# Kernel tuning notes

Hardware: AMD Instinct MI355X
Metric: run time of the kernel (lower is better)

## Reference

```python
import jax, jax.numpy as jnp
import numpy as np

W = 128    # window_size
NH = 8     # num_heads (hard-coded default in ArrowAttention/BiSPA)
NEG = -1e9


def _split_qkv(Wqkv, bqkv):
    Wq, Wk, Wv = jnp.split(Wqkv, 3, axis=1)
    bq, bk, bv = jnp.split(bqkv, 3)
    return (Wq, bq), (Wk, bk), (Wv, bv)


def cls_mha(x, Wqkv, bqkv, Wo, bo):
    # torch nn.MultiheadAttention with query = cls token, key = value = full sequence
    B, S, H = x.shape
    hd = H // NH
    (Wq, bq), (Wk, bk), (Wv, bv) = _split_qkv(Wqkv, bqkv)
    q = (x[:, :1] @ Wq + bq).reshape(B, 1, NH, hd)
    k = (x @ Wk + bk).reshape(B, S, NH, hd)
    v = (x @ Wv + bv).reshape(B, S, NH, hd)
    scores = jnp.einsum('bqhd,bkhd->bhqk', q, k) / jnp.sqrt(jnp.float32(hd))
    attn = jax.nn.softmax(scores, axis=-1)
    out = jnp.einsum('bhqk,bkhd->bqhd', attn, v).reshape(B, 1, H)
    return out @ Wo + bo


def windowed_mha(x, Wqkv, bqkv, Wo, bo, min_key):
    # Fused sliding-window MHA: token i attends to keys j with
    # max(min_key, i-W) <= j <= min(S-1, i+W). Implemented with a 3-block
    # banded layout instead of the original per-token Python loop of MHA calls.
    B, S, H = x.shape
    hd = H // NH
    (Wq, bq), (Wk, bk), (Wv, bv) = _split_qkv(Wqkv, bqkv)
    nb = (S + W - 1) // W
    Sp = nb * W
    pad = Sp - S

    def blk(t):  # [B,S,H] -> [B,nb,W,NH,hd]
        return jnp.pad(t, ((0, 0), (0, pad), (0, 0))).reshape(B, nb, W, NH, hd)

    qb = blk(x @ Wq + bq)
    kb = blk(x @ Wk + bk)
    vb = blk(x @ Wv + bv)

    def ctx(t):  # prev | cur | next block -> [B,nb,3W,NH,hd]
        tp = jnp.pad(t, ((0, 0), (1, 1), (0, 0), (0, 0), (0, 0)))
        return jnp.concatenate([tp[:, :-2], tp[:, 1:-1], tp[:, 2:]], axis=2)

    kc = ctx(kb)
    vc = ctx(vb)
    scores = jnp.einsum('bnqhd,bnkhd->bhnqk', qb, kc) / jnp.sqrt(jnp.float32(hd))
    # global positions of queries / context keys
    qpos = (jnp.arange(nb) * W)[:, None, None] + jnp.arange(W)[None, :, None]          # [nb,W,1]
    kpos = (jnp.arange(nb) * W - W)[:, None, None] + jnp.arange(3 * W)[None, None, :]  # [nb,1,3W]
    rel = kpos - qpos
    valid = (jnp.abs(rel) <= W) & (kpos >= min_key) & (kpos < S) & (qpos < S)
    scores = jnp.where(valid[None, None], scores, NEG)
    attn = jax.nn.softmax(scores, axis=-1)
    out = jnp.einsum('bhnqk,bnkhd->bnqhd', attn, vc).reshape(B, Sp, H)[:, :S]
    return out @ Wo + bo


def _sener_head(hidden_states,
                Wqkv_cls, bqkv_cls, Wo_cls, bo_cls,
                Wqkv_loc, bqkv_loc, Wo_loc, bo_loc,
                logn_scale,
                Wqkv_h, bqkv_h, Wo_h, bo_h,
                Wqkv_v, bqkv_v, Wo_v, bo_v,
                W1, b1, W2, b2, Wc, bc):
    # --- ArrowAttention ---
    global_out = cls_mha(hidden_states, Wqkv_cls, bqkv_cls, Wo_cls, bo_cls)          # [B,1,H]
    local_out = windowed_mha(hidden_states, Wqkv_loc, bqkv_loc, Wo_loc, bo_loc,
                             min_key=1)[:, 1:]                                       # [B,S-1,H]
    attended = jnp.concatenate([global_out, local_out], axis=1)                      # [B,S,H]
    # --- LogNScaling on cls token ---
    attended = jnp.concatenate([attended[:, :1] * logn_scale[0], attended[:, 1:]], axis=1)
    # --- BiSPA: two sliding-window attentions + MLP fusion ---
    h_out = windowed_mha(attended, Wqkv_h, bqkv_h, Wo_h, bo_h, min_key=0)
    v_out = windowed_mha(attended, Wqkv_v, bqkv_v, Wo_v, bo_v, min_key=0)
    combined = jnp.concatenate([h_out, v_out], axis=-1)                              # [B,S,2H]
    seq = jax.nn.relu(combined @ W1 + b1) @ W2 + b2                                  # [B,S,H]
    # dropout is identity in eval mode
    logits = seq @ Wc + bc                                                           # [B,S,L]
    return logits


def setup_inputs() -> dict:
    B, S, H, L = 2, 4096, 512, 17
    key = jax.random.key(0)
    ks = jax.random.split(key, 32)

    def p(k, shape):
        return (0.02 * jax.random.normal(k, shape)).astype(jnp.float32)

    inp = {
        'hidden_states': jax.random.normal(ks[0], (B, S, H), jnp.float32),
        'Wqkv_cls': p(ks[1], (H, 3 * H)), 'bqkv_cls': p(ks[2], (3 * H,)),
        'Wo_cls': p(ks[3], (H, H)), 'bo_cls': p(ks[4], (H,)),
        'Wqkv_loc': p(ks[5], (H, 3 * H)), 'bqkv_loc': p(ks[6], (3 * H,)),
        'Wo_loc': p(ks[7], (H, H)), 'bo_loc': p(ks[8], (H,)),
        'logn_scale': jnp.full((1,), 1.0 / np.sqrt(H), jnp.float32),
        'Wqkv_h': p(ks[9], (H, 3 * H)), 'bqkv_h': p(ks[10], (3 * H,)),
        'Wo_h': p(ks[11], (H, H)), 'bo_h': p(ks[12], (H,)),
        'Wqkv_v': p(ks[13], (H, 3 * H)), 'bqkv_v': p(ks[14], (3 * H,)),
        'Wo_v': p(ks[15], (H, H)), 'bo_v': p(ks[16], (H,)),
        'W1': p(ks[17], (2 * H, H)), 'b1': p(ks[18], (H,)),
        'W2': p(ks[19], (H, H)), 'b2': p(ks[20], (H,)),
        'Wc': p(ks[21], (H, L)), 'bc': p(ks[22], (L,)),
    }
    return inp


def reference(hidden_states,
              Wqkv_cls, bqkv_cls, Wo_cls, bo_cls,
              Wqkv_loc, bqkv_loc, Wo_loc, bo_loc,
              logn_scale,
              Wqkv_h, bqkv_h, Wo_h, bo_h,
              Wqkv_v, bqkv_v, Wo_v, bo_v,
              W1, b1, W2, b2, Wc, bc):
    return _sener_head(hidden_states,
                       Wqkv_cls, bqkv_cls, Wo_cls, bo_cls,
                       Wqkv_loc, bqkv_loc, Wo_loc, bo_loc,
                       logn_scale,
                       Wqkv_h, bqkv_h, Wo_h, bo_h,
                       Wqkv_v, bqkv_v, Wo_v, bo_v,
                       W1, b1, W2, b2, Wc, bc)
```

## Files before the change

kernel.cpp:

```cpp
#include <hip/hip_runtime.h>

#define S_ 4096
#define H_ 512
#define QKVLD 1536
#define M_ 8192
#define CCH 8

typedef __attribute__((ext_vector_type(8))) short s16x8;
typedef __attribute__((ext_vector_type(4))) float f32x4;

__device__ __forceinline__ float bflo(unsigned int w) { return __uint_as_float(w << 16); }
__device__ __forceinline__ float bfhi(unsigned int w) { return __uint_as_float(w & 0xFFFF0000u); }
__device__ __forceinline__ float bf2f(unsigned short u) { return __uint_as_float(((unsigned int)u) << 16); }
__device__ __forceinline__ unsigned short f2bf(float f) {
    unsigned int x = __float_as_uint(f);
    return (unsigned short)((x + 0x7FFFu + ((x >> 16) & 1u)) >> 16);
}
__device__ __forceinline__ void gload_lds16(const void* g, void* l) {
    __builtin_amdgcn_global_load_lds(
        (const __attribute__((address_space(1))) unsigned int*)g,
        (__attribute__((address_space(3))) unsigned int*)l, 16, 0, 0);
}

__global__ __launch_bounds__(256) void cvt_kernel(
    const float* __restrict__ in, unsigned short* __restrict__ out, int n8)
{
    int i = blockIdx.x * 256 + threadIdx.x;
    if (i >= n8) return;
    float4 a = *(const float4*)(in + (size_t)i * 8);
    float4 b = *(const float4*)(in + (size_t)i * 8 + 4);
    uint4 pk;
    pk.x = (unsigned int)f2bf(a.x) | ((unsigned int)f2bf(a.y) << 16);
    pk.y = (unsigned int)f2bf(a.z) | ((unsigned int)f2bf(a.w) << 16);
    pk.z = (unsigned int)f2bf(b.x) | ((unsigned int)f2bf(b.y) << 16);
    pk.w = (unsigned int)f2bf(b.z) | ((unsigned int)f2bf(b.w) << 16);
    *(uint4*)(out + (size_t)i * 8) = pk;
}

__global__ __launch_bounds__(256) void wtrans_kernel(
    const float* __restrict__ p0, const float* __restrict__ p1,
    const float* __restrict__ p2, const float* __restrict__ p3,
    unsigned short* o0, unsigned short* o1,
    unsigned short* o2, unsigned short* o3,
    int K, int N)
{
    const float* in; unsigned short* out;
    switch (blockIdx.z) {
        case 0:  in = p0; out = o0; break;
        case 1:  in = p1; out = o1; break;
        case 2:  in = p2; out = o2; break;
        default: in = p3; out = o3; break;
    }
    __shared__ float tile[32][33];
    int n0 = blockIdx.x * 32, k0 = blockIdx.y * 32;
    int tx = threadIdx.x & 31, ty = threadIdx.x >> 5;
    #pragma unroll
    for (int i = 0; i < 4; ++i) {
        int k = k0 + ty * 4 + i;
        tile[ty * 4 + i][tx] = in[(size_t)k * N + n0 + tx];
    }
    __syncthreads();
    #pragma unroll
    for (int i = 0; i < 4; ++i) {
        int n = n0 + ty * 4 + i;
        out[(size_t)n * K + k0 + tx] = f2bf(tile[tx][ty * 4 + i]);
    }
}

template<int BM, int RELU>
__global__ __launch_bounds__(256) void mgemm_kernel(
    const unsigned short* __restrict__ A, int lda,
    const unsigned short* __restrict__ Bt, int ldb,
    const float* __restrict__ bias,
    unsigned short* __restrict__ C, int ldc, int K)
{
    constexpr int MF = BM / 32;
    constexpr int ASEG = BM / 32;
    __shared__ __align__(16) unsigned short As[BM * 64];
    __shared__ __align__(16) unsigned short Bs[128 * 64];
    const int t = threadIdx.x;
    const int w = t >> 6, l = t & 63;
    const int wr = w >> 1, wc = w & 1;
    const int row0 = blockIdx.y * BM, col0 = blockIdx.x * 128;
    const int lr = l >> 3;
    const int lc = l & 7;

    f32x4 acc[MF][4];
    #pragma unroll
    for (int i = 0; i < MF; ++i)
        #pragma unroll
        for (int j = 0; j < 4; ++j) acc[i][j] = {0.f, 0.f, 0.f, 0.f};

    for (int k0 = 0; k0 < K; k0 += 64) {
        __syncthreads();
        #pragma unroll
        for (int i = 0; i < ASEG; ++i) {
            int seg = w * ASEG + i;
            int r = seg * 8 + lr;
            int kc = lc ^ (r & 7);
            gload_lds16(A + (size_t)(row0 + r) * lda + k0 + kc * 8,
                        (void*)(As + seg * 512));
        }
        #pragma unroll
        for (int i = 0; i < 4; ++i) {
            int seg = w * 4 + i;
            int r = seg * 8 + lr;
            int kc = lc ^ (r & 7);
            gload_lds16(Bt + (size_t)(col0 + r) * ldb + k0 + kc * 8,
                        (void*)(Bs + seg * 512));
        }
        __syncthreads();

        s16x8 af[MF][2], bf[4][2];
        #pragma unroll
        for (int mf = 0; mf < MF; ++mf)
            #pragma unroll
            for (int kk = 0; kk < 2; ++kk) {
                int r = wr * (BM / 2) + mf * 16 + (l & 15);
                int ch = (kk * 4 + (l >> 4)) ^ (r & 7);
                af[mf][kk] = *(const s16x8*)(As + r * 64 + ch * 8);
            }
        #pragma unroll
        for (int nf = 0; nf < 4; ++nf)
            #pragma unroll
            for (int kk = 0; kk < 2; ++kk) {
                int r = wc * 64 + nf * 16 + (l & 15);
                int ch = (kk * 4 + (l >> 4)) ^ (r & 7);
                bf[nf][kk] = *(const s16x8*)(Bs + r * 64 + ch * 8);
            }
        #pragma unroll
        for (int kk = 0; kk < 2; ++kk)
            #pragma unroll
            for (int mf = 0; mf < MF; ++mf)
                #pragma unroll
                for (int nf = 0; nf < 4; ++nf)
                    acc[mf][nf] = __builtin_amdgcn_mfma_f32_16x16x32_bf16(
                        af[mf][kk], bf[nf][kk], acc[mf][nf], 0, 0, 0);
    }

    #pragma unroll
    for (int mf = 0; mf < MF; ++mf)
        #pragma unroll
        for (int nf = 0; nf < 4; ++nf) {
            int col = col0 + wc * 64 + nf * 16 + (l & 15);
            float bb = bias[col];
            #pragma unroll
            for (int r4 = 0; r4 < 4; ++r4) {
                int row = row0 + wr * (BM / 2) + mf * 16 + (l >> 4) * 4 + r4;
                float v = acc[mf][nf][r4] + bb;
                if (RELU) v = fmaxf(v, 0.f);
                C[(size_t)row * ldc + col] = f2bf(v);
            }
        }
}

__global__ __launch_bounds__(256) void wattn_kernel(
    const unsigned short* __restrict__ qkv,
    unsigned short* __restrict__ out,
    int min_key)
{
    const int n = blockIdx.x, h = blockIdx.y, b = blockIdx.z;
    const int t = threadIdx.x;
    const int w = t >> 6, l = t & 63;
    const int l4 = l >> 4, lm = l & 15;

    __shared__ __align__(16) unsigned short Ks[64 * 64];
    __shared__ __align__(16) unsigned short Vt[64 * 72];
    __shared__ __align__(16) unsigned short Ps[64 * 72];

    const int q0g = n * 64;
    const size_t base = (size_t)b * S_ * QKVLD;

    s16x8 qf[2];
    {
        const unsigned short* qrow =
            qkv + base + (size_t)(q0g + w * 16 + lm) * QKVLD + h * 64 + l4 * 8;
        qf[0] = *(const s16x8*)(qrow);
        qf[1] = *(const s16x8*)(qrow + 32);
    }

    float m[4], lsum[4];
    f32x4 oacc[4];
    #pragma unroll
    for (int e = 0; e < 4; ++e) {
        m[e] = -1e30f; lsum[e] = 0.f;
        oacc[e] = {0.f, 0.f, 0.f, 0.f};
    }

    const int lr = l >> 3, lc = l & 7;

    for (int c = 0; c < 5; ++c) {
        const int klo = q0g - 128 + c * 64;
        if (klo < 0 || klo >= S_) continue;
        __syncthreads();

        #pragma unroll
        for (int i = 0; i < 2; ++i) {
            int seg = w * 2 + i;
            int r = seg * 8 + lr;
            int kc = lc ^ (r & 7);
            gload_lds16(qkv + base + (size_t)(klo + r) * QKVLD + 512 + h * 64 + kc * 8,
                        (void*)(Ks + seg * 512));
        }
        {
            int jp = (t & 31) * 2, ds = (t >> 5) * 8;
            uint4 r0 = *(const uint4*)(qkv + base + (size_t)(klo + jp) * QKVLD + 1024 + h * 64 + ds);
            uint4 r1 = *(const uint4*)(qkv + base + (size_t)(klo + jp + 1) * QKVLD + 1024 + h * 64 + ds);
            const unsigned short* va = (const unsigned short*)&r0;
            const unsigned short* vb = (const unsigned short*)&r1;
            #pragma unroll
            for (int j = 0; j < 8; ++j)
                *(unsigned int*)(Vt + (ds + j) * 72 + jp) =
                    (unsigned int)va[j] | ((unsigned int)vb[j] << 16);
        }
        __syncthreads();

        f32x4 sf[4];
        #pragma unroll
        for (int nf = 0; nf < 4; ++nf) sf[nf] = {0.f, 0.f, 0.f, 0.f};
        #pragma unroll
        for (int kk = 0; kk < 2; ++kk)
            #pragma unroll
            for (int nf = 0; nf < 4; ++nf) {
                int r = nf * 16 + lm;
                int ch = (kk * 4 + l4) ^ (r & 7);
                s16x8 kf = *(const s16x8*)(Ks + r * 64 + ch * 8);
                sf[nf] = __builtin_amdgcn_mfma_f32_16x16x32_bf16(qf[kk], kf, sf[nf], 0, 0, 0);
            }

        #pragma unroll
        for (int r4 = 0; r4 < 4; ++r4) {
            const int qpos = q0g + w * 16 + l4 * 4 + r4;
            float sv[4];
            #pragma unroll
            for (int nf = 0; nf < 4; ++nf) {
                int kpos = klo + nf * 16 + lm;
                int rel = kpos - qpos;
                bool valid = (rel <= 128) & (rel >= -128) & (kpos >= min_key);
                sv[nf] = valid ? sf[nf][r4] * 0.125f : -1e9f;
            }
            float mx = fmaxf(fmaxf(sv[0], sv[1]), fmaxf(sv[2], sv[3]));
            #pragma unroll
            for (int st = 1; st < 16; st <<= 1)
                mx = fmaxf(mx, __shfl_xor(mx, st, 64));
            float mn = fmaxf(m[r4], mx);
            float sc = __expf(m[r4] - mn);
            float ps = 0.f;
            #pragma unroll
            for (int nf = 0; nf < 4; ++nf) {
                sv[nf] = __expf(sv[nf] - mn);
                ps += sv[nf];
            }
            #pragma unroll
            for (int st = 1; st < 16; st <<= 1)
                ps += __shfl_xor(ps, st, 64);
            lsum[r4] = lsum[r4] * sc + ps;
            m[r4] = mn;
            #pragma unroll
            for (int nf = 0; nf < 4; ++nf) oacc[nf][r4] *= sc;
            const int prow = w * 16 + l4 * 4 + r4;
            #pragma unroll
            for (int nf = 0; nf < 4; ++nf)
                Ps[prow * 72 + nf * 16 + lm] = f2bf(sv[nf]);
        }

        #pragma unroll
        for (int kk = 0; kk < 2; ++kk) {
            s16x8 pf = *(const s16x8*)(Ps + (w * 16 + lm) * 72 + l4 * 8 + kk * 32);
            #pragma unroll
            for (int nf = 0; nf < 4; ++nf) {
                s16x8 vf = *(const s16x8*)(Vt + (nf * 16 + lm) * 72 + l4 * 8 + kk * 32);
                oacc[nf] = __builtin_amdgcn_mfma_f32_16x16x32_bf16(pf, vf, oacc[nf], 0, 0, 0);
            }
        }
    }

    #pragma unroll
    for (int r4 = 0; r4 < 4; ++r4) {
        float inv = 1.f / lsum[r4];
        size_t row = (size_t)b * S_ + q0g + w * 16 + l4 * 4 + r4;
        #pragma unroll
        for (int nf = 0; nf < 4; ++nf)
            out[row * H_ + h * 64 + nf * 16 + lm] = f2bf(oacc[nf][r4] * inv);
    }
}

__global__ __launch_bounds__(256) void qcls_kernel(
    const unsigned short* __restrict__ xb, const unsigned short* __restrict__ WqkvT,
    const float* __restrict__ bqkv, float* __restrict__ q_cls)
{
    int gw = blockIdx.x * 4 + (threadIdx.x >> 6);
    int l = threadIdx.x & 63;
    int b = gw >> 9, j = gw & 511;
    s16x8 xv = *(const s16x8*)(xb + (size_t)b * S_ * H_ + l * 8);
    s16x8 wv = *(const s16x8*)(WqkvT + (size_t)j * 512 + l * 8);
    float s = 0.f;
    #pragma unroll
    for (int e = 0; e < 8; ++e)
        s += bf2f((unsigned short)xv[e]) * bf2f((unsigned short)wv[e]);
    #pragma unroll
    for (int st = 1; st < 64; st <<= 1) s += __shfl_xor(s, st, 64);
    if (l == 0) q_cls[gw] = s + bqkv[j];
}

__global__ __launch_bounds__(256) void cls_attn_part(
    const float* __restrict__ q_cls, const unsigned short* __restrict__ qkv,
    float* __restrict__ part)
{
    const int bh = blockIdx.x, ck = blockIdx.y;
    const int b = bh >> 3, h = bh & 7;
    const int t = threadIdx.x;
    __shared__ float sQ[64];
    __shared__ float sP[512];
    __shared__ float red[256];
    __shared__ float pacc[16][64];
    if (t < 64) sQ[t] = q_cls[b * H_ + h * 64 + t] * 0.125f;
    __syncthreads();
    const size_t base = (size_t)b * S_ * QKVLD;
    const int j0 = ck * 512;

    float sv[2], smax = -1e30f;
    #pragma unroll
    for (int i = 0; i < 2; ++i) {
        int j = j0 + t + i * 256;
        const unsigned short* kr = qkv + base + (size_t)j * QKVLD + 512 + h * 64;
        float s = 0.f;
        #pragma unroll
        for (int d8 = 0; d8 < 8; ++d8) {
            uint4 raw = *(const uint4*)(kr + d8 * 8);
            const float* q = &sQ[d8 * 8];
            s = fmaf(q[0], bflo(raw.x), s); s = fmaf(q[1], bfhi(raw.x), s);
            s = fmaf(q[2], bflo(raw.y), s); s = fmaf(q[3], bfhi(raw.y), s);
            s = fmaf(q[4], bflo(raw.z), s); s = fmaf(q[5], bfhi(raw.z), s);
            s = fmaf(q[6], bflo(raw.w), s); s = fmaf(q[7], bfhi(raw.w), s);
        }
        sv[i] = s;
        smax = fmaxf(smax, s);
    }
    red[t] = smax; __syncthreads();
    for (int st = 128; st > 0; st >>= 1) {
        if (t < st) red[t] = fmaxf(red[t], red[t + st]);
        __syncthreads();
    }
    float mc = red[0];
    __syncthreads();
    float ls = 0.f;
    #pragma unroll
    for (int i = 0; i < 2; ++i) {
        float p = __expf(sv[i] - mc);
        sP[t + i * 256] = p;
        ls += p;
    }
    red[t] = ls; __syncthreads();
    for (int st = 128; st > 0; st >>= 1) {
        if (t < st) red[t] += red[t + st];
        __syncthreads();
    }
    float lc = red[0];

    int g = t >> 4, d4 = t & 15;
    float4 acc; acc.x = 0.f; acc.y = 0.f; acc.z = 0.f; acc.w = 0.f;
    for (int j = g * 32; j < g * 32 + 32; ++j) {
        float p = sP[j];
        uint2 raw = *(const uint2*)(qkv + base + (size_t)(j0 + j) * QKVLD + 1024 + h * 64 + d4 * 4);
        acc.x = fmaf(p, bflo(raw.x), acc.x); acc.y = fmaf(p, bfhi(raw.x), acc.y);
        acc.z = fmaf(p, bflo(raw.y), acc.z); acc.w = fmaf(p, bfhi(raw.y), acc.w);
    }
    *(float4*)&pacc[g][d4 * 4] = acc;
    __syncthreads();
    float* op = part + (size_t)(bh * CCH + ck) * 66;
    if (t < 64) {
        float r = 0.f;
        #pragma unroll
        for (int g2 = 0; g2 < 16; ++g2) r += pacc[g2][t];
        op[t] = r;
    }
    if (t == 64) op[64] = mc;
    if (t == 65) op[65] = lc;
}

__global__ __launch_bounds__(64) void cls_attn_reduce(
    const float* __restrict__ part, float* __restrict__ gpre)
{
    int bh = blockIdx.x, t = threadIdx.x;
    int b = bh >> 3, h = bh & 7;
    const float* pp = part + (size_t)bh * CCH * 66;
    float M = -1e30f;
    #pragma unroll
    for (int c = 0; c < CCH; ++c) M = fmaxf(M, pp[c * 66 + 64]);
    float L = 0.f, o = 0.f;
    #pragma unroll
    for (int c = 0; c < CCH; ++c) {
        float wgt = __expf(pp[c * 66 + 64] - M);
        L += pp[c * 66 + 65] * wgt;
        o += pp[c * 66 + t] * wgt;
    }
    gpre[b * H_ + h * 64 + t] = o / L;
}

__global__ __launch_bounds__(256) void clsproj_kernel(
    const float* __restrict__ gpre, const unsigned short* __restrict__ WoT,
    const float* __restrict__ bo, const float* __restrict__ logn,
    unsigned short* __restrict__ attended)
{
    int gw = blockIdx.x * 4 + (threadIdx.x >> 6);
    int l = threadIdx.x & 63;
    int b = gw >> 9, j = gw & 511;
    const float* gr = gpre + b * H_ + l * 8;
    s16x8 wv = *(const s16x8*)(WoT + (size_t)j * 512 + l * 8);
    float s = 0.f;
    #pragma unroll
    for (int e = 0; e < 8; ++e) s += gr[e] * bf2f((unsigned short)wv[e]);
    #pragma unroll
    for (int st = 1; st < 64; st <<= 1) s += __shfl_xor(s, st, 64);
    if (l == 0) attended[(size_t)b * S_ * H_ + j] = f2bf((s + bo[j]) * logn[0]);
}

__global__ __launch_bounds__(256) void logits_kernel(
    const unsigned short* __restrict__ seq, const float* __restrict__ Wc,
    const float* __restrict__ bc, float* __restrict__ out)
{
    __shared__ float sWc[17][516];
    for (int i = threadIdx.x; i < 512 * 17; i += 256) {
        int d = i / 17, lcol = i % 17;
        sWc[lcol][d] = Wc[i];
    }
    __syncthreads();
    int idx = blockIdx.x * 256 + threadIdx.x;
    if (idx >= M_ * 17) return;
    int r = idx / 17, lcol = idx % 17;
    const unsigned short* sr = seq + (size_t)r * H_;
    float s = bc[lcol];
    for (int d8 = 0; d8 < 64; ++d8) {
        uint4 raw = *(const uint4*)(sr + d8 * 8);
        const float* wr = &sWc[lcol][d8 * 8];
        s = fmaf(bflo(raw.x), wr[0], s); s = fmaf(bfhi(raw.x), wr[1], s);
        s = fmaf(bflo(raw.y), wr[2], s); s = fmaf(bfhi(raw.y), wr[3], s);
        s = fmaf(bflo(raw.z), wr[4], s); s = fmaf(bfhi(raw.z), wr[5], s);
        s = fmaf(bflo(raw.w), wr[6], s); s = fmaf(bfhi(raw.w), wr[7], s);
    }
    out[idx] = s;
}

extern "C" void kernel_launch(void* const* d_in, const int* in_sizes, int n_in,
                              void* d_out, int out_size, void* d_ws, size_t ws_size,
                              hipStream_t stream) {
    const float* x        = (const float*)d_in[0];
    const float* Wqkv_cls = (const float*)d_in[1];
    const float* bqkv_cls = (const float*)d_in[2];
    const float* Wo_cls   = (const float*)d_in[3];
    const float* bo_cls   = (const float*)d_in[4];
    const float* Wqkv_loc = (const float*)d_in[5];
    const float* bqkv_loc = (const float*)d_in[6];
    const float* Wo_loc   = (const float*)d_in[7];
    const float* bo_loc   = (const float*)d_in[8];
    const float* logn     = (const float*)d_in[9];
    const float* Wqkv_h   = (const float*)d_in[10];
    const float* bqkv_h   = (const float*)d_in[11];
    const float* Wo_h     = (const float*)d_in[12];
    const float* bo_h     = (const float*)d_in[13];
    const float* Wqkv_v   = (const float*)d_in[14];
    const float* bqkv_v   = (const float*)d_in[15];
    const float* Wo_v     = (const float*)d_in[16];
    const float* bo_v     = (const float*)d_in[17];
    const float* W1       = (const float*)d_in[18];
    const float* b1       = (const float*)d_in[19];
    const float* W2       = (const float*)d_in[20];
    const float* b2       = (const float*)d_in[21];
    const float* Wc       = (const float*)d_in[22];
    const float* bc       = (const float*)d_in[23];
    float* out = (float*)d_out;

    unsigned short* wsu = (unsigned short*)d_ws;
    unsigned short* xb        = wsu;
    unsigned short* qkv       = wsu +  8388608;
    unsigned short* attnout   = wsu + 20971520;
    unsigned short* attended  = wsu + 25165824;
    unsigned short* combined  = wsu + 29360128;
    unsigned short* hidden    = wsu + 37748736;
    unsigned short* seq       = wsu + 41943040;
    unsigned short* WqkvT_cls = wsu + 46137344;
    unsigned short* WqkvT_loc = wsu + 46923776;
    unsigned short* WqkvT_h   = wsu + 47710208;
    unsigned short* WqkvT_v   = wsu + 48496640;
    unsigned short* WoT_loc   = wsu + 49283072;
    unsigned short* WoT_h     = wsu + 49545216;
    unsigned short* WoT_v     = wsu + 49807360;
    unsigned short* W2T       = wsu + 50069504;
    unsigned short* W1T       = wsu + 50331648;
    unsigned short* WoT_cls   = wsu + 50855936;
    float* q_cls              = (float*)(wsu + 51118080);
    float* gpre               = q_cls + 1024;
    float* part               = gpre + 1024;

    dim3 blk(256);

    cvt_kernel<<<dim3(2048), blk, 0, stream>>>(x, xb, 524288);
    wtrans_kernel<<<dim3(48, 16, 4), blk, 0, stream>>>(
        Wqkv_cls, Wqkv_loc, Wqkv_h, Wqkv_v,
        WqkvT_cls, WqkvT_loc, WqkvT_h, WqkvT_v, 512, 1536);
    wtrans_kernel<<<dim3(16, 16, 4), blk, 0, stream>>>(
        Wo_loc, Wo_h, Wo_v, W2, WoT_loc, WoT_h, WoT_v, W2T, 512, 512);
    wtrans_kernel<<<dim3(16, 32, 1), blk, 0, stream>>>(
        W1, W1, W1, W1, W1T, W1T, W1T, W1T, 1024, 512);
    wtrans_kernel<<<dim3(16, 16, 1), blk, 0, stream>>>(
        Wo_cls, Wo_cls, Wo_cls, Wo_cls, WoT_cls, WoT_cls, WoT_cls, WoT_cls, 512, 512);

    mgemm_kernel<128, 0><<<dim3(8, 64), blk, 0, stream>>>(
        xb, 512, WqkvT_cls + 512 * 512, 512, bqkv_cls + 512, qkv + 512, 1536, 512);
    qcls_kernel<<<dim3(256), blk, 0, stream>>>(xb, WqkvT_cls, bqkv_cls, q_cls);
    cls_attn_part<<<dim3(16, CCH), blk, 0, stream>>>(q_cls, qkv, part);
    cls_attn_reduce<<<dim3(16), dim3(64), 0, stream>>>(part, gpre);

    mgemm_kernel<128, 0><<<dim3(12, 64), blk, 0, stream>>>(
        xb, 512, WqkvT_loc, 512, bqkv_loc, qkv, 1536, 512);
    wattn_kernel<<<dim3(64, 8, 2), blk, 0, stream>>>(qkv, attnout, 1);
    mgemm_kernel<64, 0><<<dim3(4, 128), blk, 0, stream>>>(
        attnout, 512, WoT_loc, 512, bo_loc, attended, 512, 512);
    clsproj_kernel<<<dim3(256), blk, 0, stream>>>(gpre, WoT_cls, bo_cls, logn, attended);

    mgemm_kernel<128, 0><<<dim3(12, 64), blk, 0, stream>>>(
        attended, 512, WqkvT_h, 512, bqkv_h, qkv, 1536, 512);
    wattn_kernel<<<dim3(64, 8, 2), blk, 0, stream>>>(qkv, attnout, 0);
    mgemm_kernel<64, 0><<<dim3(4, 128), blk, 0, stream>>>(
        attnout, 512, WoT_h, 512, bo_h, combined, 1024, 512);

    mgemm_kernel<128, 0><<<dim3(12, 64), blk, 0, stream>>>(
        attended, 512, WqkvT_v, 512, bqkv_v, qkv, 1536, 512);
    wattn_kernel<<<dim3(64, 8, 2), blk, 0, stream>>>(qkv, attnout, 0);
    mgemm_kernel<64, 0><<<dim3(4, 128), blk, 0, stream>>>(
        attnout, 512, WoT_v, 512, bo_v, combined + 512, 1024, 512);

    mgemm_kernel<64, 1><<<dim3(4, 128), blk, 0, stream>>>(
        combined, 1024, W1T, 1024, b1, hidden, 512, 1024);
    mgemm_kernel<64, 0><<<dim3(4, 128), blk, 0, stream>>>(
        hidden, 512, W2T, 512, b2, seq, 512, 512);
    logits_kernel<<<dim3((M_ * 17 + 255) / 256), blk, 0, stream>>>(seq, Wc, bc, out);
}
```

Baseline: 358.4 us.

## Batch sibling QKV projections, attention and output GEMMs into wider launches

Merges the cls K/V and local QKV projections into one GEMM writing a 2560-wide buffer. The h and v branch QKV projections become one 3072-wide GEMM, and a single attention launch with a doubled z grid covers both branches. The two output projections become one z-batched GEMM, and the cls weight transpose is folded into an existing launch. Attention also skips mask arithmetic for interior key chunks. The aim is fewer kernel launches and better GPU fill, at the cost of extra workspace and per-column bias selection in the GEMM epilogue.

```diff
diff --git a/kernel.cpp b/kernel.cpp
--- a/kernel.cpp
+++ b/kernel.cpp
@@ -2,7 +2,6 @@
 
 #define S_ 4096
 #define H_ 512
-#define QKVLD 1536
 #define M_ 8192
 #define CCH 8
 
@@ -40,8 +39,9 @@
 __global__ __launch_bounds__(256) void wtrans_kernel(
     const float* __restrict__ p0, const float* __restrict__ p1,
     const float* __restrict__ p2, const float* __restrict__ p3,
+    const float* __restrict__ p4,
     unsigned short* o0, unsigned short* o1,
-    unsigned short* o2, unsigned short* o3,
+    unsigned short* o2, unsigned short* o3, unsigned short* o4,
     int K, int N)
 {
     const float* in; unsigned short* out;
@@ -49,7 +49,8 @@
         case 0:  in = p0; out = o0; break;
         case 1:  in = p1; out = o1; break;
         case 2:  in = p2; out = o2; break;
-        default: in = p3; out = o3; break;
+        case 3:  in = p3; out = o3; break;
+        default: in = p4; out = o4; break;
     }
     __shared__ float tile[32][33];
     int n0 = blockIdx.x * 32, k0 = blockIdx.y * 32;
@@ -71,13 +72,19 @@
 __global__ __launch_bounds__(256) void mgemm_kernel(
     const unsigned short* __restrict__ A, int lda,
     const unsigned short* __restrict__ Bt, int ldb,
-    const float* __restrict__ bias,
-    unsigned short* __restrict__ C, int ldc, int K)
+    const float* __restrict__ bias, const float* __restrict__ biasB, int nsplit,
+    unsigned short* __restrict__ C, int ldc, int K,
+    size_t az, size_t bz, size_t cz)
 {
     constexpr int MF = BM / 32;
     constexpr int ASEG = BM / 32;
     __shared__ __align__(16) unsigned short As[BM * 64];
     __shared__ __align__(16) unsigned short Bs[128 * 64];
+    const int z = blockIdx.z;
+    A  += (size_t)z * az;
+    Bt += (size_t)z * bz;
+    C  += (size_t)z * cz;
+    if (z > 0) bias = biasB;
     const int t = threadIdx.x;
     const int w = t >> 6, l = t & 63;
     const int wr = w >> 1, wc = w & 1;
@@ -143,7 +150,7 @@
         #pragma unroll
         for (int nf = 0; nf < 4; ++nf) {
             int col = col0 + wc * 64 + nf * 16 + (l & 15);
-            float bb = bias[col];
+            float bb = (col < nsplit) ? bias[col] : biasB[col - nsplit];
             #pragma unroll
             for (int r4 = 0; r4 < 4; ++r4) {
                 int row = row0 + wr * (BM / 2) + mf * 16 + (l >> 4) * 4 + r4;
@@ -155,11 +162,11 @@
 }
 
 __global__ __launch_bounds__(256) void wattn_kernel(
-    const unsigned short* __restrict__ qkv,
-    unsigned short* __restrict__ out,
-    int min_key)
-{
-    const int n = blockIdx.x, h = blockIdx.y, b = blockIdx.z;
+    const unsigned short* __restrict__ qkv, int qld, int qbase,
+    unsigned short* __restrict__ out, size_t brstride, int min_key)
+{
+    const int n = blockIdx.x, h = blockIdx.y;
+    const int z = blockIdx.z, br = z >> 1, b = z & 1;
     const int t = threadIdx.x;
     const int w = t >> 6, l = t & 63;
     const int l4 = l >> 4, lm = l & 15;
@@ -169,12 +176,14 @@
     __shared__ __align__(16) unsigned short Ps[64 * 72];
 
     const int q0g = n * 64;
-    const size_t base = (size_t)b * S_ * QKVLD;
+    const int qcol = qbase + br * 1536;
+    const size_t base = (size_t)b * S_ * qld;
+    out += (size_t)br * brstride;
 
     s16x8 qf[2];
     {
         const unsigned short* qrow =
-            qkv + base + (size_t)(q0g + w * 16 + lm) * QKVLD + h * 64 + l4 * 8;
+            qkv + base + (size_t)(q0g + w * 16 + lm) * qld + qcol + h * 64 + l4 * 8;
         qf[0] = *(const s16x8*)(qrow);
         qf[1] = *(const s16x8*)(qrow + 32);
     }
@@ -192,6 +201,7 @@
     for (int c = 0; c < 5; ++c) {
         const int klo = q0g - 128 + c * 64;
         if (klo < 0 || klo >= S_) continue;
+        const bool need_mask = (c == 0) | (c == 4) | (klo < min_key);
         __syncthreads();
 
         #pragma unroll
@@ -199,13 +209,13 @@
             int seg = w * 2 + i;
             int r = seg * 8 + lr;
             int kc = lc ^ (r & 7);
-            gload_lds16(qkv + base + (size_t)(klo + r) * QKVLD + 512 + h * 64 + kc * 8,
+            gload_lds16(qkv + base + (size_t)(klo + r) * qld + qcol + 512 + h * 64 + kc * 8,
                         (void*)(Ks + seg * 512));
         }
         {
             int jp = (t & 31) * 2, ds = (t >> 5) * 8;
-            uint4 r0 = *(const uint4*)(qkv + base + (size_t)(klo + jp) * QKVLD + 1024 + h * 64 + ds);
-            uint4 r1 = *(const uint4*)(qkv + base + (size_t)(klo + jp + 1) * QKVLD + 1024 + h * 64 + ds);
+            uint4 r0 = *(const uint4*)(qkv + base + (size_t)(klo + jp) * qld + qcol + 1024 + h * 64 + ds);
+            uint4 r1 = *(const uint4*)(qkv + base + (size_t)(klo + jp + 1) * qld + qcol + 1024 + h * 64 + ds);
             const unsigned short* va = (const unsigned short*)&r0;
             const unsigned short* vb = (const unsigned short*)&r1;
             #pragma unroll
@@ -233,11 +243,15 @@
             const int qpos = q0g + w * 16 + l4 * 4 + r4;
             float sv[4];
             #pragma unroll
-            for (int nf = 0; nf < 4; ++nf) {
-                int kpos = klo + nf * 16 + lm;
-                int rel = kpos - qpos;
-                bool valid = (rel <= 128) & (rel >= -128) & (kpos >= min_key);
-                sv[nf] = valid ? sf[nf][r4] * 0.125f : -1e9f;
+            for (int nf = 0; nf < 4; ++nf) sv[nf] = sf[nf][r4] * 0.125f;
+            if (need_mask) {
+                #pragma unroll
+                for (int nf = 0; nf < 4; ++nf) {
+                    int kpos = klo + nf * 16 + lm;
+                    int rel = kpos - qpos;
+                    bool valid = (rel <= 128) & (rel >= -128) & (kpos >= min_key);
+                    if (!valid) sv[nf] = -1e9f;
+                }
             }
             float mx = fmaxf(fmaxf(sv[0], sv[1]), fmaxf(sv[2], sv[3]));
             #pragma unroll
@@ -281,7 +295,7 @@
         size_t row = (size_t)b * S_ + q0g + w * 16 + l4 * 4 + r4;
         #pragma unroll
         for (int nf = 0; nf < 4; ++nf)
-            out[row * H_ + h * 64 + nf * 16 + lm] = f2bf(oacc[nf][r4] * inv);
+            out[row * 512 + h * 64 + nf * 16 + lm] = f2bf(oacc[nf][r4] * inv);
     }
 }
 
@@ -316,14 +330,14 @@
     __shared__ float pacc[16][64];
     if (t < 64) sQ[t] = q_cls[b * H_ + h * 64 + t] * 0.125f;
     __syncthreads();
-    const size_t base = (size_t)b * S_ * QKVLD;
+    const size_t base = (size_t)b * S_ * 2560;
     const int j0 = ck * 512;
 
     float sv[2], smax = -1e30f;
     #pragma unroll
     for (int i = 0; i < 2; ++i) {
         int j = j0 + t + i * 256;
-        const unsigned short* kr = qkv + base + (size_t)j * QKVLD + 512 + h * 64;
+        const unsigned short* kr = qkv + base + (size_t)j * 2560 + h * 64;
         float s = 0.f;
         #pragma unroll
         for (int d8 = 0; d8 < 8; ++d8) {
@@ -362,7 +376,7 @@
     float4 acc; acc.x = 0.f; acc.y = 0.f; acc.z = 0.f; acc.w = 0.f;
     for (int j = g * 32; j < g * 32 + 32; ++j) {
         float p = sP[j];
-        uint2 raw = *(const uint2*)(qkv + base + (size_t)(j0 + j) * QKVLD + 1024 + h * 64 + d4 * 4);
+        uint2 raw = *(const uint2*)(qkv + base + (size_t)(j0 + j) * 2560 + 512 + h * 64 + d4 * 4);
         acc.x = fmaf(p, bflo(raw.x), acc.x); acc.y = fmaf(p, bfhi(raw.x), acc.y);
         acc.z = fmaf(p, bflo(raw.y), acc.z); acc.w = fmaf(p, bfhi(raw.y), acc.w);
     }
@@ -473,67 +487,71 @@
 
     unsigned short* wsu = (unsigned short*)d_ws;
     unsigned short* xb        = wsu;
-    unsigned short* qkv       = wsu +  8388608;
-    unsigned short* attnout   = wsu + 20971520;
-    unsigned short* attended  = wsu + 25165824;
-    unsigned short* combined  = wsu + 29360128;
-    unsigned short* hidden    = wsu + 37748736;
-    unsigned short* seq       = wsu + 41943040;
-    unsigned short* WqkvT_cls = wsu + 46137344;
-    unsigned short* WqkvT_loc = wsu + 46923776;
-    unsigned short* WqkvT_h   = wsu + 47710208;
-    unsigned short* WqkvT_v   = wsu + 48496640;
-    unsigned short* WoT_loc   = wsu + 49283072;
-    unsigned short* WoT_h     = wsu + 49545216;
-    unsigned short* WoT_v     = wsu + 49807360;
-    unsigned short* W2T       = wsu + 50069504;
-    unsigned short* W1T       = wsu + 50331648;
-    unsigned short* WoT_cls   = wsu + 50855936;
-    float* q_cls              = (float*)(wsu + 51118080);
+    unsigned short* qkvA      = wsu +  4194304;
+    unsigned short* qkvB      = wsu + 25165824;
+    unsigned short* attnout_h = wsu + 50331648;
+    unsigned short* attnout_v = wsu + 54525952;
+    unsigned short* attended  = wsu + 58720256;
+    unsigned short* combined  = wsu + 62914560;
+    unsigned short* hidden    = wsu + 71303168;
+    unsigned short* seq       = attended;
+    unsigned short* WqkvT_cls = wsu + 75497472;
+    unsigned short* WqkvT_loc = wsu + 76283904;
+    unsigned short* WqkvT_h   = wsu + 77070336;
+    unsigned short* WqkvT_v   = wsu + 77856768;
+    unsigned short* WoT_loc   = wsu + 78643200;
+    unsigned short* WoT_h     = wsu + 78905344;
+    unsigned short* WoT_v     = wsu + 79167488;
+    unsigned short* W2T       = wsu + 79429632;
+    unsigned short* W1T       = wsu + 79691776;
+    unsigned short* WoT_cls   = wsu + 80216064;
+    float* q_cls              = (float*)(wsu + 80478208);
     float* gpre               = q_cls + 1024;
     float* part               = gpre + 1024;
 
+    const int NSP_NONE = 1 << 30;
     dim3 blk(256);
 
     cvt_kernel<<<dim3(2048), blk, 0, stream>>>(x, xb, 524288);
     wtrans_kernel<<<dim3(48, 16, 4), blk, 0, stream>>>(
-        Wqkv_cls, Wqkv_loc, Wqkv_h, Wqkv_v,
-        WqkvT_cls, WqkvT_loc, WqkvT_h, WqkvT_v, 512, 1536);
-    wtrans_kernel<<<dim3(16, 16, 4), blk, 0, stream>>>(
-        Wo_loc, Wo_h, Wo_v, W2, WoT_loc, WoT_h, WoT_v, W2T, 512, 512);
+        Wqkv_cls, Wqkv_loc, Wqkv_h, Wqkv_v, Wqkv_cls,
+        WqkvT_cls, WqkvT_loc, WqkvT_h, WqkvT_v, WqkvT_cls, 512, 1536);
+    wtrans_kernel<<<dim3(16, 16, 5), blk, 0, stream>>>(
+        Wo_loc, Wo_h, Wo_v, W2, Wo_cls,
+        WoT_loc, WoT_h, WoT_v, W2T, WoT_cls, 512, 512);
     wtrans_kernel<<<dim3(16, 32, 1), blk, 0, stream>>>(
-        W1, W1, W1, W1, W1T, W1T, W1T, W1T, 1024, 512);
-    wtrans_kernel<<<dim3(16, 16, 1), blk, 0, stream>>>(
-        Wo_cls, Wo_cls, Wo_cls, Wo_cls, WoT_cls, WoT_cls, WoT_cls, WoT_cls, 512, 512);
-
-    mgemm_kernel<128, 0><<<dim3(8, 64), blk, 0, stream>>>(
-        xb, 512, WqkvT_cls + 512 * 512, 512, bqkv_cls + 512, qkv + 512, 1536, 512);
+        W1, W1, W1, W1, W1,
+        W1T, W1T, W1T, W1T, W1T, 1024, 512);
+
+    mgemm_kernel<128, 0><<<dim3(20, 64), blk, 0, stream>>>(
+        xb, 512, WqkvT_cls + 512 * 512, 512,
+        bqkv_cls + 512, bqkv_loc, 1024, qkvA, 2560, 512, 0, 0, 0);
+
     qcls_kernel<<<dim3(256), blk, 0, stream>>>(xb, WqkvT_cls, bqkv_cls, q_cls);
-    cls_attn_part<<<dim3(16, CCH), blk, 0, stream>>>(q_cls, qkv, part);
+    cls_attn_part<<<dim3(16, CCH), blk, 0, stream>>>(q_cls, qkvA, part);
     cls_attn_reduce<<<dim3(16), dim3(64), 0, stream>>>(part, gpre);
 
-    mgemm_kernel<128, 0><<<dim3(12, 64), blk, 0, stream>>>(
-        xb, 512, WqkvT_loc, 512, bqkv_loc, qkv, 1536, 512);
-    wattn_kernel<<<dim3(64, 8, 2), blk, 0, stream>>>(qkv, attnout, 1);
+    wattn_kernel<<<dim3(64, 8, 2), blk, 0, stream>>>(
+        qkvA, 2560, 1024, attnout_h, 0, 1);
     mgemm_kernel<64, 0><<<dim3(4, 128), blk, 0, stream>>>(
-        attnout, 512, WoT_loc, 512, bo_loc, attended, 512, 512);
+        attnout_h, 512, WoT_loc, 512, bo_loc, bo_loc, NSP_NONE,
+        attended, 512, 512, 0, 0, 0);
     clsproj_kernel<<<dim3(256), blk, 0, stream>>>(gpre, WoT_cls, bo_cls, logn, attended);
 
-    mgemm_kernel<128, 0><<<dim3(12, 64), blk, 0, stream>>>(
-        attended, 512, WqkvT_h, 512, bqkv_h, qkv, 1536, 512);
-    wattn_kernel<<<dim3(64, 8, 2), blk, 0, stream>>>(qkv, attnout, 0);
+    mgemm_kernel<128, 0><<<dim3(24, 64), blk, 0, stream>>>(
+        attended, 512, WqkvT_h, 512,
+        bqkv_h, bqkv_v, 1536, qkvB, 3072, 512, 0, 0, 0);
+
+    wattn_kernel<<<dim3(64, 8, 4), blk, 0, stream>>>(
+        qkvB, 3072, 0, attnout_h, 4194304, 0);
+
+    mgemm_kernel<64, 0><<<dim3(4, 128, 2), blk, 0, stream>>>(
+        attnout_h, 512, WoT_h, 512, bo_h, bo_v, NSP_NONE,
+        combined, 1024, 512, 4194304, 262144, 512);
+
+    mgemm_kernel<64, 1><<<dim3(4, 128), blk, 0, stream>>>(
+        combined, 1024, W1T, 1024, b1, b1, NSP_NONE, hidden, 512, 1024, 0, 0, 0);
     mgemm_kernel<64, 0><<<dim3(4, 128), blk, 0, stream>>>(
-        attnout, 512, WoT_h, 512, bo_h, combined, 1024, 512);
-
-    mgemm_kernel<128, 0><<<dim3(12, 64), blk, 0, stream>>>(
-        attended, 512, WqkvT_v, 512, bqkv_v, qkv, 1536, 512);
-    wattn_kernel<<<dim3(64, 8, 2), blk, 0, stream>>>(qkv, attnout, 0);
-    mgemm_kernel<64, 0><<<dim3(4, 128), blk, 0, stream>>>(
-        attnout, 512, WoT_v, 512, bo_v, combined + 512, 1024, 512);
-
-    mgemm_kernel<64, 1><<<dim3(4, 128), blk, 0, stream>>>(
-        combined, 1024, W1T, 1024, b1, hidden, 512, 1024);
-    mgemm_kernel<64, 0><<<dim3(4, 128), blk, 0, stream>>>(
-        hidden, 512, W2T, 512, b2, seq, 512, 512);
+        hidden, 512, W2T, 512, b2, b2, NSP_NONE, seq, 512, 512, 0, 0, 0);
     logits_kernel<<<dim3((M_ * 17 + 255) / 256), blk, 0, stream>>>(seq, Wc, bc, out);
 }
```

Result: faster. 336.4 us (-6.1%).
